# Kernel optimization log

Measured on AMD Instinct MI355X. Metric: run time of the kernel, lower is better.

The kernel has to match this reference:

```python
import jax, jax.numpy as jnp
import numpy as np

_OFF = [(dz, dy, dx) for dz in (-1, 0, 1) for dy in (-1, 0, 1) for dx in (-1, 0, 1)]
_K3 = [(kz, ky, kx) for kz in range(3) for ky in range(3) for kx in range(3)]


def _key(c, dims):
    D, H, W = dims
    return ((c[:, 0].astype(np.int64) * D + c[:, 1]) * H + c[:, 2]) * W + c[:, 3]


def _dedupe(c, dims):
    k = _key(c, dims)
    _, idx = np.unique(k, return_index=True)
    return c[np.sort(idx)]


def _make_lookup(coords, dims):
    D, H, W = dims
    keys = _key(coords, dims)
    order = np.argsort(keys)
    skeys = keys[order]

    def query(qc):
        valid = ((qc[:, 1] >= 0) & (qc[:, 1] < D) & (qc[:, 2] >= 0) & (qc[:, 2] < H)
                 & (qc[:, 3] >= 0) & (qc[:, 3] < W))
        qk = _key(np.where(valid[:, None], qc, 0), dims)
        pos = np.clip(np.searchsorted(skeys, qk), 0, len(skeys) - 1)
        hit = valid & (skeys[pos] == qk)
        return np.where(hit, order[pos], -1).astype(np.int32)
    return query


def _subm_nbr(coords, query):
    nbr = np.empty((len(coords), 27), np.int32)
    for ki, (dz, dy, dx) in enumerate(_OFF):
        qc = coords.copy()
        qc[:, 1] += dz; qc[:, 2] += dy; qc[:, 3] += dx
        nbr[:, ki] = query(qc)
    return nbr


def _down(in_coords, pads, out_dims, in_query):
    # spconv SparseConv3d k=3 s=2: output active set + gather rulebook (in = 2*out - p + k)
    p = np.array(pads)
    cand = []
    for k in _K3:
        t = in_coords[:, 1:] + p - np.array(k)
        m = (t % 2 == 0).all(1)
        o = t[m] // 2
        ok = (o >= 0).all(1) & (o < np.array(out_dims)).all(1)
        cand.append(np.concatenate([in_coords[m][ok][:, :1], o[ok]], 1))
    out_coords = _dedupe(np.concatenate(cand), out_dims)
    nbrd = np.empty((len(out_coords), 27), np.int32)
    for ki, k in enumerate(_K3):
        qc = out_coords.copy()
        qc[:, 1:] = out_coords[:, 1:] * 2 - p + np.array(k)
        nbrd[:, ki] = in_query(qc)
    return out_coords, nbrd


def _inv(in_coords, pads, out_query):
    # inverse conv: for each stride-s input voxel i, gather downsampled voxel o = (i+p-k)/2
    p = np.array(pads)
    nbr = np.full((len(in_coords), 27), -1, np.int32)
    for ki, k in enumerate(_K3):
        t = in_coords[:, 1:] + p - np.array(k)
        div = (t % 2 == 0).all(1)
        qc = in_coords.copy()
        qc[:, 1:] = np.where(div[:, None], t // 2, -1)
        nbr[:, ki] = np.where(div, out_query(qc), -1)
    return nbr


def setup_inputs() -> dict:
    rng = np.random.default_rng(0)
    B, K, P, STD = 4, 160, 128, 3.0
    D1 = (41, 1024, 1024)  # sparse_shape (z, y, x)
    pts = []
    for b in range(B):
        ctr = np.stack([rng.uniform(2, d - 3, K) for d in D1], 1)
        pb = ctr[:, None, :] + rng.normal(0.0, STD, (K, P, 3))
        pb = np.clip(np.rint(pb.reshape(-1, 3)), 0, np.array(D1) - 1).astype(np.int64)
        pts.append(np.concatenate([np.full((len(pb), 1), b, np.int64), pb], 1))
    c1 = _dedupe(np.concatenate(pts), D1)
    D2 = tuple((d + 2 * q - 3) // 2 + 1 for d, q in zip(D1, (1, 1, 1)))
    D3 = tuple((d + 2 * q - 3) // 2 + 1 for d, q in zip(D2, (1, 1, 1)))
    D4 = tuple((d + 2 * q - 3) // 2 + 1 for d, q in zip(D3, (0, 1, 1)))
    q1 = _make_lookup(c1, D1); nbr1 = _subm_nbr(c1, q1)
    c2, nbrd2 = _down(c1, (1, 1, 1), D2, q1); q2 = _make_lookup(c2, D2); nbr2 = _subm_nbr(c2, q2)
    c3, nbrd3 = _down(c2, (1, 1, 1), D3, q2); q3 = _make_lookup(c3, D3); nbr3 = _subm_nbr(c3, q3)
    c4, nbrd4 = _down(c3, (0, 1, 1), D4, q3); q4 = _make_lookup(c4, D4); nbr4 = _subm_nbr(c4, q4)
    nbri4 = _inv(c3, (0, 1, 1), q4)
    nbri3 = _inv(c2, (1, 1, 1), q3)
    nbri2 = _inv(c1, (1, 1, 1), q2)
    N1 = len(c1)
    w = lambda *s: jnp.asarray((0.05 * rng.standard_normal(s)).astype(np.float32))
    bn = lambda n, c: jnp.asarray(np.stack([1.0 + 0.02 * rng.standard_normal((n, c)),
                                            0.02 * rng.standard_normal((n, c))], 1).astype(np.float32))
    return {
        'voxel_feat': jnp.asarray(rng.standard_normal((N1, 4)).astype(np.float32)),
        'Win': w(27, 4, 32),
        'W32': w(10, 27, 32, 32),
        'W64': w(10, 27, 64, 64),
        'Wd3': w(27, 32, 64),
        'W6432': w(3, 27, 64, 32),
        'W12864': w(2, 27, 128, 64),
        'bn32': bn(14, 32),
        'bn64': bn(13, 64),
        'nbr1': jnp.asarray(nbr1), 'nbr2': jnp.asarray(nbr2),
        'nbr3': jnp.asarray(nbr3), 'nbr4': jnp.asarray(nbr4),
        'nbrd2': jnp.asarray(nbrd2), 'nbrd3': jnp.asarray(nbrd3), 'nbrd4': jnp.asarray(nbrd4),
        'nbri4': jnp.asarray(nbri4), 'nbri3': jnp.asarray(nbri3), 'nbri2': jnp.asarray(nbri2),
    }


def _conv(feat, nbr, W):
    # rulebook gather-matmul-scatter: out[n] = sum_k feat[nbr[n,k]] @ W[k]
    out = jnp.zeros((nbr.shape[0], W.shape[-1]), feat.dtype)
    for k in range(27):
        idx = nbr[:, k]
        g = jnp.where((idx >= 0)[:, None], feat[jnp.maximum(idx, 0)], 0.0)
        out = out + g @ W[k]
    return out


def _block(f, nbr, W, sb):  # conv + (folded, eval-mode) BN + ReLU
    return jax.nn.relu(_conv(f, nbr, W) * sb[0] + sb[1])


def _basic(f, nbr, Wa, sa, Wb, sb):  # SparseBasicBlock
    h = jax.nn.relu(_conv(f, nbr, Wa) * sa[0] + sa[1])
    h = _conv(h, nbr, Wb) * sb[0] + sb[1]
    return jax.nn.relu(h + f)


def _reduce(c, oc):  # channel_reduction: view(n, oc, -1).sum(2)
    return c.reshape(c.shape[0], oc, -1).sum(-1)


def _forward(voxel_feat, Win, W32, W64, Wd3, W6432, W12864, bn32, bn64,
             nbr1, nbr2, nbr3, nbr4, nbrd2, nbrd3, nbrd4, nbri4, nbri3, nbri2):
    x = _block(voxel_feat, nbr1, Win, bn32[0])       # conv_input
    x1 = _block(x, nbr1, W32[0], bn32[1])            # conv1
    h = _block(x1, nbrd2, W32[1], bn32[2])           # spconv2 stride-2
    h = _block(h, nbr2, W32[2], bn32[3])
    x2 = _block(h, nbr2, W32[3], bn32[4])
    h = _block(x2, nbrd3, Wd3, bn64[0])              # spconv3 stride-2, 32->64
    h = _block(h, nbr3, W64[0], bn64[1])
    x3 = _block(h, nbr3, W64[1], bn64[2])
    h = _block(x3, nbrd4, W64[2], bn64[3])           # spconv4 stride-2, pad (0,1,1)
    h = _block(h, nbr4, W64[3], bn64[4])
    x4 = _block(h, nbr4, W64[4], bn64[5])
    # UR block 4 (lateral = bottom = x4)
    t = _basic(x4, nbr4, W64[5], bn64[6], W64[6], bn64[7])
    cat = jnp.concatenate([x4, t], 1)                # [N4, 128]
    x = _block(cat, nbr4, W12864[0], bn64[11]) + _reduce(cat, 64)
    xu4 = _block(x, nbri4, W64[7], bn64[8])          # inverseconv -> level 3
    # UR block 3
    t = _basic(x3, nbr3, W64[8], bn64[9], W64[9], bn64[10])
    cat = jnp.concatenate([xu4, t], 1)
    x = _block(cat, nbr3, W12864[1], bn64[12]) + _reduce(cat, 64)
    xu3 = _block(x, nbri3, W6432[0], bn32[11])       # inverseconv -> level 2, 32ch
    # UR block 2
    t = _basic(x2, nbr2, W32[4], bn32[5], W32[5], bn32[6])
    cat = jnp.concatenate([xu3, t], 1)
    x = _block(cat, nbr2, W6432[1], bn32[12]) + _reduce(cat, 32)
    xu2 = _block(x, nbri2, W32[6], bn32[7])          # inverseconv -> level 1
    # UR block 1 (conv_inv = conv5, submanifold at level 1)
    t = _basic(x1, nbr1, W32[7], bn32[8], W32[8], bn32[9])
    cat = jnp.concatenate([xu2, t], 1)
    x = _block(cat, nbr1, W6432[2], bn32[13]) + _reduce(cat, 32)
    return _block(x, nbr1, W32[9], bn32[10])         # conv5 -> unet_voxel_feat [N1, 32]


def reference(voxel_feat, Win, W32, W64, Wd3, W6432, W12864, bn32, bn64,
              nbr1, nbr2, nbr3, nbr4, nbrd2, nbrd3, nbrd4, nbri4, nbri3, nbri2):
    return _forward(voxel_feat, Win, W32, W64, Wd3, W6432, W12864, bn32, bn64,
                    nbr1, nbr2, nbr3, nbr4, nbrd2, nbrd3, nbrd4, nbri4, nbri3, nbri2)
```

## Files before the change

### kernel.cpp

```cpp
#include <hip/hip_runtime.h>


template<int CIN_A, int CIN_B, int COUT, int EPI, bool SPLIT>
__global__ __launch_bounds__(256) void spconv(
    const float* __restrict__ inA,
    const float* __restrict__ inB,
    const int*   __restrict__ nbr,
    const float* __restrict__ W,
    const float* __restrict__ bn,
    const float* __restrict__ skip,
    float*       __restrict__ out,
    float*       __restrict__ pout,
    int N, int KS)
{
    constexpr int CIN = CIN_A + CIN_B;
    constexpr int NQ  = COUT / 4;

    const int lane = threadIdx.x & 63;
    const int wid  = threadIdx.x >> 6;

    unsigned nwg = gridDim.x;
    unsigned q8 = nwg / 8u, r8 = nwg % 8u;
    unsigned xcd = blockIdx.x % 8u, sub = blockIdx.x / 8u;
    unsigned id = (xcd < r8 ? xcd * (q8 + 1u) : r8 * (q8 + 1u) + (xcd - r8) * q8) + sub;

    int kg, rb;
    if (SPLIT) { kg = (int)(id % (unsigned)KS); rb = (int)(id / (unsigned)KS); }
    else       { kg = 0;  rb = (int)id; }
    const int kper = SPLIT ? 27 / KS : 27;
    const int k0 = kg * kper, k1 = k0 + kper;

    const int row = rb * 256 + wid * 64 + lane;
    const bool rv = row < N;
    const int* nbrp = nbr + (size_t)row * 27;

    float4 acc[NQ];
    #pragma unroll
    for (int q = 0; q < NQ; ++q) acc[q] = make_float4(0.f, 0.f, 0.f, 0.f);

    int idx = rv ? nbrp[k0] : -1;
    for (int k = k0; k < k1; ++k) {
        const int nidx = (rv && k + 1 < k1) ? nbrp[k + 1] : -1;
        const float* wb = W + (size_t)k * CIN * COUT;
        const float  mk = (idx >= 0) ? 1.f : 0.f;
        const int    si = (idx >= 0) ? idx : 0;

        auto do4 = [&](float4 g, const float* wci) {
            g.x *= mk; g.y *= mk; g.z *= mk; g.w *= mk;
            #pragma unroll
            for (int j = 0; j < 4; ++j) {
                const float gv = (&g.x)[j];
                const float4* wr = (const float4*)(wci + j * COUT);
                #pragma unroll
                for (int q = 0; q < NQ; ++q) {
                    float4 w = wr[q];
                    acc[q].x += gv * w.x; acc[q].y += gv * w.y;
                    acc[q].z += gv * w.z; acc[q].w += gv * w.w;
                }
            }
        };

        const float* rA = inA + (size_t)si * CIN_A;
        #pragma unroll 2
        for (int c4 = 0; c4 < CIN_A / 4; ++c4)
            do4(*(const float4*)(rA + c4 * 4), wb + (size_t)(c4 * 4) * COUT);
        if (CIN_B > 0) {
            const float* rB = inB + (size_t)si * CIN_B;
            #pragma unroll 2
            for (int c4 = 0; c4 < CIN_B / 4; ++c4)
                do4(*(const float4*)(rB + c4 * 4), wb + (size_t)(CIN_A + c4 * 4) * COUT);
        }
        idx = nidx;
    }

    if (SPLIT) {
        if (rv) {
            float* pp = pout + ((size_t)kg * N + row) * COUT;
            #pragma unroll
            for (int q = 0; q < NQ; ++q) *(float4*)(pp + q * 4) = acc[q];
        }
        return;
    }
    if (!rv) return;

    float*       op   = out + (size_t)row * COUT;
    const float* skp  = (EPI == 1) ? skip + (size_t)row * COUT : nullptr;
    const float* catA = inA + (size_t)row * CIN_A;
    const float* catB = (CIN_B > 0) ? inB + (size_t)row * CIN_B : nullptr;

    #pragma unroll
    for (int q = 0; q < NQ; ++q) {
        float4 sc = *(const float4*)(bn + q * 4);
        float4 bi = *(const float4*)(bn + COUT + q * 4);
        float4 y;
        y.x = acc[q].x * sc.x + bi.x;
        y.y = acc[q].y * sc.y + bi.y;
        y.z = acc[q].z * sc.z + bi.z;
        y.w = acc[q].w * sc.w + bi.w;
        if (EPI == 1) {
            float4 s = *(const float4*)(skp + q * 4);
            y.x += s.x; y.y += s.y; y.z += s.z; y.w += s.w;
        }
        y.x = fmaxf(y.x, 0.f); y.y = fmaxf(y.y, 0.f);
        y.z = fmaxf(y.z, 0.f); y.w = fmaxf(y.w, 0.f);
        if (EPI == 2) {
            const float* rs = (8 * q < CIN_A) ? catA + 8 * q : catB + 8 * q - CIN_A;
            float4 p0 = ((const float4*)rs)[0];
            float4 p1 = ((const float4*)rs)[1];
            y.x += p0.x + p0.y; y.y += p0.z + p0.w;
            y.z += p1.x + p1.y; y.w += p1.z + p1.w;
        }
        *(float4*)(op + q * 4) = y;
    }
}

template<int CIN_A, int CIN_B, int COUT, int EPI>
__global__ __launch_bounds__(256) void epi_k(
    const float* __restrict__ P, int KS,
    const float* __restrict__ bn,
    const float* __restrict__ skip,
    const float* __restrict__ inA,
    const float* __restrict__ inB,
    float* __restrict__ out, int N)
{
    int t = blockIdx.x * 256 + threadIdx.x;
    int total = N * (COUT / 4);
    if (t >= total) return;
    int r   = t / (COUT / 4);
    int co0 = (t % (COUT / 4)) * 4;

    float4 y = make_float4(0.f, 0.f, 0.f, 0.f);
    for (int kg = 0; kg < KS; ++kg) {
        float4 p = *(const float4*)(P + ((size_t)kg * N + r) * COUT + co0);
        y.x += p.x; y.y += p.y; y.z += p.z; y.w += p.w;
    }
    float4 sc = *(const float4*)(bn + co0);
    float4 bi = *(const float4*)(bn + COUT + co0);
    y.x = y.x * sc.x + bi.x; y.y = y.y * sc.y + bi.y;
    y.z = y.z * sc.z + bi.z; y.w = y.w * sc.w + bi.w;
    if (EPI == 1) {
        float4 s = *(const float4*)(skip + (size_t)r * COUT + co0);
        y.x += s.x; y.y += s.y; y.z += s.z; y.w += s.w;
    }
    y.x = fmaxf(y.x, 0.f); y.y = fmaxf(y.y, 0.f);
    y.z = fmaxf(y.z, 0.f); y.w = fmaxf(y.w, 0.f);
    if (EPI == 2) {
        const float* rs = (2 * co0 < CIN_A)
            ? inA + (size_t)r * CIN_A + 2 * co0
            : inB + (size_t)r * CIN_B + 2 * co0 - CIN_A;
        float4 p0 = ((const float4*)rs)[0];
        float4 p1 = ((const float4*)rs)[1];
        y.x += p0.x + p0.y; y.y += p0.z + p0.w;
        y.z += p1.x + p1.y; y.w += p1.z + p1.w;
    }
    *(float4*)(out + (size_t)r * COUT + co0) = y;
}

static inline int ksel(int nblk, int N, int CO, size_t prem_elems) {
    int ks = 27;
    if (nblk >= 600) ks = 1;
    else if (nblk * 3 >= 600) ks = 3;
    else if (nblk * 9 >= 600) ks = 9;
    while (ks > 1 && (size_t)ks * (size_t)N * (size_t)CO > prem_elems) ks /= 3;
    return ks;
}

extern "C" void kernel_launch(void* const* d_in, const int* in_sizes, int n_in,
                              void* d_out, int out_size, void* d_ws, size_t ws_size,
                              hipStream_t stream)
{
    (void)n_in; (void)out_size;
    const float* vf     = (const float*)d_in[0];
    const float* Win    = (const float*)d_in[1];
    const float* W32    = (const float*)d_in[2];
    const float* W64    = (const float*)d_in[3];
    const float* Wd3    = (const float*)d_in[4];
    const float* W6432  = (const float*)d_in[5];
    const float* W12864 = (const float*)d_in[6];
    const float* bn32   = (const float*)d_in[7];
    const float* bn64   = (const float*)d_in[8];
    const int* nbr1  = (const int*)d_in[9];
    const int* nbr2  = (const int*)d_in[10];
    const int* nbr3  = (const int*)d_in[11];
    const int* nbr4  = (const int*)d_in[12];
    const int* nbrd2 = (const int*)d_in[13];
    const int* nbrd3 = (const int*)d_in[14];
    const int* nbrd4 = (const int*)d_in[15];
    const int* nbri4 = (const int*)d_in[16];
    const int* nbri3 = (const int*)d_in[17];
    const int* nbri2 = (const int*)d_in[18];

    const int N1 = in_sizes[9]  / 27;
    const int N2 = in_sizes[10] / 27;
    const int N3 = in_sizes[11] / 27;
    const int N4 = in_sizes[12] / 27;

    float* ws = (float*)d_ws;
    size_t off = 0;
    auto alloc = [&](size_t n) { float* p = ws + off; off += n; return p; };
    float* X1  = alloc((size_t)N1 * 32);
    float* TA  = alloc((size_t)N1 * 32);
    float* TA2 = alloc((size_t)N1 * 32);
    float* TU1 = alloc((size_t)N1 * 32);
    float* X2  = alloc((size_t)N2 * 32);
    float* TB2 = alloc((size_t)N2 * 32);
    float* TC2 = alloc((size_t)N2 * 32);
    float* TU2 = alloc((size_t)N2 * 32);
    float* X3  = alloc((size_t)N3 * 64);
    float* TB3 = alloc((size_t)N3 * 64);
    float* TC3 = alloc((size_t)N3 * 64);
    float* TU3 = alloc((size_t)N3 * 64);
    float* X4  = alloc((size_t)N4 * 64);
    float* TB4 = alloc((size_t)N4 * 64);
    float* TC4 = alloc((size_t)N4 * 64);
    float* OUT = (float*)d_out;

    size_t prem = (ws_size / 4 > off + 1024) ? (ws_size / 4 - off - 1024) : 0;
    float* P = ws + off;

    const size_t S32 = 27*32*32, S64 = (size_t)27*64*64, S6432 = (size_t)27*64*32, S12864 = (size_t)27*128*64;

#define CONV(CA, CB, CO, EP, pA, pB, pN, pW, pBN, pS, pO, NN) do {                      \
        int nblk_ = ((NN) + 255) / 256;                                                 \
        int ks_ = ksel(nblk_, (NN), (CO), prem);                                        \
        if (ks_ == 1) {                                                                 \
            spconv<CA, CB, CO, EP, false><<<dim3((unsigned)nblk_), 256, 0, stream>>>(   \
                pA, pB, pN, pW, pBN, pS, pO, nullptr, NN, 1);                           \
        } else {                                                                        \
            spconv<CA, CB, CO, EP, true><<<dim3((unsigned)(nblk_ * ks_)), 256, 0, stream>>>( \
                pA, pB, pN, pW, pBN, pS, nullptr, P, NN, ks_);                          \
            int tot4_ = (NN) * ((CO) / 4);                                              \
            epi_k<CA, CB, CO, EP><<<dim3((unsigned)((tot4_ + 255) / 256)), 256, 0, stream>>>( \
                P, ks_, pBN, pS, pA, pB, pO, NN);                                       \
        }                                                                               \
    } while (0)

    CONV(4,0,32,0,  vf,  nullptr, nbr1,  Win,         bn32+0*64,  nullptr, TA,  N1);
    CONV(32,0,32,0, TA,  nullptr, nbr1,  W32+0*S32,   bn32+1*64,  nullptr, X1,  N1);
    CONV(32,0,32,0, X1,  nullptr, nbrd2, W32+1*S32,   bn32+2*64,  nullptr, TB2, N2);
    CONV(32,0,32,0, TB2, nullptr, nbr2,  W32+2*S32,   bn32+3*64,  nullptr, TC2, N2);
    CONV(32,0,32,0, TC2, nullptr, nbr2,  W32+3*S32,   bn32+4*64,  nullptr, X2,  N2);
    CONV(32,0,64,0, X2,  nullptr, nbrd3, Wd3,         bn64+0*128, nullptr, TB3, N3);
    CONV(64,0,64,0, TB3, nullptr, nbr3,  W64+0*S64,   bn64+1*128, nullptr, TC3, N3);
    CONV(64,0,64,0, TC3, nullptr, nbr3,  W64+1*S64,   bn64+2*128, nullptr, X3,  N3);
    CONV(64,0,64,0, X3,  nullptr, nbrd4, W64+2*S64,   bn64+3*128, nullptr, TB4, N4);
    CONV(64,0,64,0, TB4, nullptr, nbr4,  W64+3*S64,   bn64+4*128, nullptr, TC4, N4);
    CONV(64,0,64,0, TC4, nullptr, nbr4,  W64+4*S64,   bn64+5*128, nullptr, X4,  N4);
    CONV(64,0,64,0, X4,  nullptr, nbr4,  W64+5*S64,   bn64+6*128, nullptr, TB4, N4);
    CONV(64,0,64,1, TB4, nullptr, nbr4,  W64+6*S64,   bn64+7*128, X4,      TC4, N4);
    CONV(64,64,64,2, X4, TC4,     nbr4,  W12864+0*S12864, bn64+11*128, nullptr, TB4, N4);
    CONV(64,0,64,0, TB4, nullptr, nbri4, W64+7*S64,   bn64+8*128, nullptr, TU3, N3);
    CONV(64,0,64,0, X3,  nullptr, nbr3,  W64+8*S64,   bn64+9*128, nullptr, TB3, N3);
    CONV(64,0,64,1, TB3, nullptr, nbr3,  W64+9*S64,   bn64+10*128, X3,     TC3, N3);
    CONV(64,64,64,2, TU3, TC3,    nbr3,  W12864+1*S12864, bn64+12*128, nullptr, TB3, N3);
    CONV(64,0,32,0, TB3, nullptr, nbri3, W6432+0*S6432, bn32+11*64, nullptr, TU2, N2);
    CONV(32,0,32,0, X2,  nullptr, nbr2,  W32+4*S32,   bn32+5*64,  nullptr, TB2, N2);
    CONV(32,0,32,1, TB2, nullptr, nbr2,  W32+5*S32,   bn32+6*64,  X2,      TC2, N2);
    CONV(32,32,32,2, TU2, TC2,    nbr2,  W6432+1*S6432, bn32+12*64, nullptr, TB2, N2);
    CONV(32,0,32,0, TB2, nullptr, nbri2, W32+6*S32,   bn32+7*64,  nullptr, TU1, N1);
    CONV(32,0,32,0, X1,  nullptr, nbr1,  W32+7*S32,   bn32+8*64,  nullptr, TA,  N1);
    CONV(32,0,32,1, TA,  nullptr, nbr1,  W32+8*S32,   bn32+9*64,  X1,      TA2, N1);
    CONV(32,32,32,2, TU1, TA2,    nbr1,  W6432+2*S6432, bn32+13*64, nullptr, TA,  N1);
    CONV(32,0,32,0, TA,  nullptr, nbr1,  W32+9*S32,   bn32+10*64, nullptr, OUT, N1);
#undef CONV
}
```

Measured before the change: 4.630 ms.

## Load conv weights via scalar s_load into SGPRs and skip empty offsets per wave

```diff
diff --git a/kernel.cpp b/kernel.cpp
--- a/kernel.cpp
+++ b/kernel.cpp
@@ -1,5 +1,7 @@
 #include <hip/hip_runtime.h>
 
+
+typedef float f32x16 __attribute__((ext_vector_type(16)));
 
 template<int CIN_A, int CIN_B, int COUT, int EPI, bool SPLIT>
 __global__ __launch_bounds__(256) void spconv(
@@ -13,11 +15,13 @@
     float*       __restrict__ pout,
     int N, int KS)
 {
-    constexpr int CIN = CIN_A + CIN_B;
-    constexpr int NQ  = COUT / 4;
-
-    const int lane = threadIdx.x & 63;
-    const int wid  = threadIdx.x >> 6;
+    constexpr int CIN   = CIN_A + CIN_B;
+    constexpr int CHUNK = (CIN >= 32) ? 32 : CIN;
+    constexpr int NCHK  = CIN / CHUNK;
+    constexpr int GV    = CHUNK / 4;
+    constexpr int NSTEP = CHUNK * COUT / 64;
+
+    const int tid = threadIdx.x;
 
     unsigned nwg = gridDim.x;
     unsigned q8 = nwg / 8u, r8 = nwg % 8u;
@@ -30,45 +34,76 @@
     const int kper = SPLIT ? 27 / KS : 27;
     const int k0 = kg * kper, k1 = k0 + kper;
 
-    const int row = rb * 256 + wid * 64 + lane;
-    const bool rv = row < N;
+    const int  row = rb * 256 + tid;
+    const bool rv  = row < N;
     const int* nbrp = nbr + (size_t)row * 27;
 
-    float4 acc[NQ];
+    float acc[COUT];
     #pragma unroll
-    for (int q = 0; q < NQ; ++q) acc[q] = make_float4(0.f, 0.f, 0.f, 0.f);
+    for (int i = 0; i < COUT; ++i) acc[i] = 0.f;
 
     int idx = rv ? nbrp[k0] : -1;
     for (int k = k0; k < k1; ++k) {
         const int nidx = (rv && k + 1 < k1) ? nbrp[k + 1] : -1;
-        const float* wb = W + (size_t)k * CIN * COUT;
-        const float  mk = (idx >= 0) ? 1.f : 0.f;
-        const int    si = (idx >= 0) ? idx : 0;
-
-        auto do4 = [&](float4 g, const float* wci) {
-            g.x *= mk; g.y *= mk; g.z *= mk; g.w *= mk;
-            #pragma unroll
-            for (int j = 0; j < 4; ++j) {
-                const float gv = (&g.x)[j];
-                const float4* wr = (const float4*)(wci + j * COUT);
+        if (__ballot(idx >= 0) != 0ull) {
+            const float mk = (idx >= 0) ? 1.f : 0.f;
+            const int   si = (idx >= 0) ? idx : 0;
+            const float* wk = W + (size_t)k * (CIN * COUT);
+
+            #pragma unroll 1
+            for (int c = 0; c < NCHK; ++c) {
+                const float* src;
+                if constexpr (CIN_B == 0)
+                    src = inA + (size_t)si * CIN_A + c * CHUNK;
+                else
+                    src = (c * CHUNK < CIN_A)
+                        ? inA + (size_t)si * CIN_A + c * CHUNK
+                        : inB + (size_t)si * CIN_B + (c * CHUNK - CIN_A);
+                float4 g[GV];
                 #pragma unroll
-                for (int q = 0; q < NQ; ++q) {
-                    float4 w = wr[q];
-                    acc[q].x += gv * w.x; acc[q].y += gv * w.y;
-                    acc[q].z += gv * w.z; acc[q].w += gv * w.w;
+                for (int v = 0; v < GV; ++v) g[v] = ((const float4*)src)[v];
+                #pragma unroll
+                for (int v = 0; v < GV; ++v) {
+                    g[v].x *= mk; g[v].y *= mk; g[v].z *= mk; g[v].w *= mk;
+                }
+
+                const float* wkc = wk + c * (CHUNK * COUT);
+                #pragma unroll
+                for (int ss = 0; ss < NSTEP; ++ss) {
+                    const float* wp = wkc + ss * 64;
+                    f32x16 w0, w1, w2, w3;
+                    asm volatile("s_load_dwordx16 %0, %1, 0x0"  : "=s"(w0) : "s"(wp));
+                    asm volatile("s_load_dwordx16 %0, %1, 0x40" : "=s"(w1) : "s"(wp));
+                    asm volatile("s_load_dwordx16 %0, %1, 0x80" : "=s"(w2) : "s"(wp));
+                    asm volatile("s_load_dwordx16 %0, %1, 0xc0" : "=s"(w3) : "s"(wp));
+                    asm volatile("s_waitcnt lgkmcnt(0)"
+                                 : "+s"(w0), "+s"(w1), "+s"(w2), "+s"(w3));
+                    if constexpr (COUT == 64) {
+                        const int ci = ss;
+                        const float gv = ((const float*)&g[ci >> 2])[ci & 3];
+                        #pragma unroll
+                        for (int q = 0; q < 16; ++q) acc[q]      += gv * w0[q];
+                        #pragma unroll
+                        for (int q = 0; q < 16; ++q) acc[16 + q] += gv * w1[q];
+                        #pragma unroll
+                        for (int q = 0; q < 16; ++q) acc[32 + q] += gv * w2[q];
+                        #pragma unroll
+                        for (int q = 0; q < 16; ++q) acc[48 + q] += gv * w3[q];
+                    } else {
+                        const int ci0 = 2 * ss, ci1 = 2 * ss + 1;
+                        const float gv0 = ((const float*)&g[ci0 >> 2])[ci0 & 3];
+                        const float gv1 = ((const float*)&g[ci1 >> 2])[ci1 & 3];
+                        #pragma unroll
+                        for (int q = 0; q < 16; ++q) acc[q]      += gv0 * w0[q];
+                        #pragma unroll
+                        for (int q = 0; q < 16; ++q) acc[16 + q] += gv0 * w1[q];
+                        #pragma unroll
+                        for (int q = 0; q < 16; ++q) acc[q]      += gv1 * w2[q];
+                        #pragma unroll
+                        for (int q = 0; q < 16; ++q) acc[16 + q] += gv1 * w3[q];
+                    }
                 }
             }
-        };
-
-        const float* rA = inA + (size_t)si * CIN_A;
-        #pragma unroll 2
-        for (int c4 = 0; c4 < CIN_A / 4; ++c4)
-            do4(*(const float4*)(rA + c4 * 4), wb + (size_t)(c4 * 4) * COUT);
-        if (CIN_B > 0) {
-            const float* rB = inB + (size_t)si * CIN_B;
-            #pragma unroll 2
-            for (int c4 = 0; c4 < CIN_B / 4; ++c4)
-                do4(*(const float4*)(rB + c4 * 4), wb + (size_t)(CIN_A + c4 * 4) * COUT);
         }
         idx = nidx;
     }
@@ -77,7 +112,8 @@
         if (rv) {
             float* pp = pout + ((size_t)kg * N + row) * COUT;
             #pragma unroll
-            for (int q = 0; q < NQ; ++q) *(float4*)(pp + q * 4) = acc[q];
+            for (int q = 0; q < COUT / 4; ++q)
+                *(float4*)(pp + q * 4) = make_float4(acc[4*q], acc[4*q+1], acc[4*q+2], acc[4*q+3]);
         }
         return;
     }
@@ -89,14 +125,14 @@
     const float* catB = (CIN_B > 0) ? inB + (size_t)row * CIN_B : nullptr;
 
     #pragma unroll
-    for (int q = 0; q < NQ; ++q) {
+    for (int q = 0; q < COUT / 4; ++q) {
         float4 sc = *(const float4*)(bn + q * 4);
         float4 bi = *(const float4*)(bn + COUT + q * 4);
         float4 y;
-        y.x = acc[q].x * sc.x + bi.x;
-        y.y = acc[q].y * sc.y + bi.y;
-        y.z = acc[q].z * sc.z + bi.z;
-        y.w = acc[q].w * sc.w + bi.w;
+        y.x = acc[4*q+0] * sc.x + bi.x;
+        y.y = acc[4*q+1] * sc.y + bi.y;
+        y.z = acc[4*q+2] * sc.z + bi.z;
+        y.w = acc[4*q+3] * sc.w + bi.w;
         if (EPI == 1) {
             float4 s = *(const float4*)(skp + q * 4);
             y.x += s.x; y.y += s.y; y.z += s.z; y.w += s.w;
@@ -158,9 +194,9 @@
 
 static inline int ksel(int nblk, int N, int CO, size_t prem_elems) {
     int ks = 27;
-    if (nblk >= 600) ks = 1;
-    else if (nblk * 3 >= 600) ks = 3;
-    else if (nblk * 9 >= 600) ks = 9;
+    if (nblk >= 640) ks = 1;
+    else if (nblk * 3 >= 640) ks = 3;
+    else if (nblk * 9 >= 640) ks = 9;
     while (ks > 1 && (size_t)ks * (size_t)N * (size_t)CO > prem_elems) ks /= 3;
     return ks;
 }
```

Measured after the change: 4.438 ms. -4.2%, faster.
